# Kernel tuning notes

Hardware: AMD Instinct MI355X
Metric: run time of the kernel (lower is better)

Reference implementation:

```python
import jax, jax.numpy as jnp
import numpy as np

B, LQ, LK = 4, 512, 512
QS, KS, H, DV = 512, 512, 256, 512


def setup_inputs() -> dict:
    key = jax.random.key(0)
    ks = jax.random.split(key, 9)
    s_q = 1.0 / np.sqrt(QS)
    s_k = 1.0 / np.sqrt(KS)
    s_v = 1.0 / np.sqrt(H)
    return {
        "query": jax.random.normal(ks[0], (B, LQ, QS), jnp.float32),
        "key": jax.random.normal(ks[1], (B, LK, KS), jnp.float32),
        "value": jax.random.normal(ks[2], (B, LK, DV), jnp.float32),
        "wq": jax.random.uniform(ks[3], (H, QS), jnp.float32, -s_q, s_q),
        "bq": jax.random.uniform(ks[4], (H,), jnp.float32, -s_q, s_q),
        "wk": jax.random.uniform(ks[5], (H, KS), jnp.float32, -s_k, s_k),
        "bk": jax.random.uniform(ks[6], (H,), jnp.float32, -s_k, s_k),
        "wv": jax.random.uniform(ks[7], (H,), jnp.float32, -s_v, s_v),
        "bv": jax.random.uniform(ks[8], (), jnp.float32, -s_v, s_v),
    }


def reference(query, key, value, wq, bq, wk, bk, wv, bv):
    # q: [B, Lq, H], k: [B, Lk, H]
    q = jnp.einsum('bqd,hd->bqh', query, wq) + bq
    k = jnp.einsum('bkd,hd->bkh', key, wk) + bk
    # broadcast add -> [B, Lq, Lk, H], tanh, project to scalar score
    feats = jnp.tanh(q[:, :, None, :] + k[:, None, :, :])
    scores = jnp.einsum('bqkh,h->bqk', feats, wv) + bv  # [B, Lq, Lk]
    attn = jax.nn.softmax(scores, axis=-1)
    # dropout p=0.0 (identity at inference)
    return jnp.einsum('bqk,bkd->bqd', attn, value)
```

## Files before the change

### kernel.cpp

```cpp
#include <hip/hip_runtime.h>

#define LOG2E 1.4426950408889634f

constexpr int Bb = 4, LQ = 512, LK = 512, QS = 512, H = 256, DV = 512;
constexpr int M = 2048;

constexpr size_t OFF_EQT = 0;
constexpr size_t OFF_EKT = 2u << 20;
constexpr size_t OFF_PQ  = 4u << 20;
constexpr size_t OFF_ROW = 6u << 20;

using bf16x8 = __attribute__((ext_vector_type(8))) short;
using f32x4v = __attribute__((ext_vector_type(4))) float;

__device__ inline unsigned short f2bf(float x) {
    unsigned int u = __float_as_uint(x);
    u += 0x7FFFu + ((u >> 16) & 1u);
    return (unsigned short)(u >> 16);
}
__device__ inline unsigned int pk2(float lo, float hi) {
    return (unsigned int)f2bf(lo) | ((unsigned int)f2bf(hi) << 16);
}

__global__ __launch_bounds__(256) void proj_mfma(
    const float* __restrict__ query, const float* __restrict__ key,
    const float* __restrict__ wq, const float* __restrict__ wk,
    const float* __restrict__ bq, const float* __restrict__ bk,
    char* __restrict__ ws, float scale)
{
    const int z = blockIdx.z;
    const float* A    = z ? key : query;
    const float* W    = z ? wk : wq;
    const float* bias = z ? bk : bq;
    float* out = (float*)(ws + (z ? OFF_EKT : OFF_EQT));

    __shared__ unsigned short Als[64][136];
    __shared__ unsigned short Wls[64][136];
    __shared__ float Ot[64][68];

    const int mb = blockIdx.x * 64, nb = blockIdx.y * 64;
    const int tid = threadIdx.x;
    const int wid = tid >> 6, lane = tid & 63;
    const int ml = lane & 15, quad = lane >> 4;

    f32x4v acc[4] = {{0,0,0,0},{0,0,0,0},{0,0,0,0},{0,0,0,0}};

    for (int kc = 0; kc < QS; kc += 128) {
        __syncthreads();
#pragma unroll
        for (int it = 0; it < 4; ++it) {
            int u = tid + it * 256;
            int row = u >> 4, c8 = (u & 15) * 8;
            float4 a0 = *(const float4*)(A + (size_t)(mb + row) * 512 + kc + c8);
            float4 a1 = *(const float4*)(A + (size_t)(mb + row) * 512 + kc + c8 + 4);
            uint4 pa = { pk2(a0.x, a0.y), pk2(a0.z, a0.w), pk2(a1.x, a1.y), pk2(a1.z, a1.w) };
            *(uint4*)&Als[row][c8] = pa;
            float4 w0 = *(const float4*)(W + (size_t)(nb + row) * 512 + kc + c8);
            float4 w1 = *(const float4*)(W + (size_t)(nb + row) * 512 + kc + c8 + 4);
            uint4 pw = { pk2(w0.x, w0.y), pk2(w0.z, w0.w), pk2(w1.x, w1.y), pk2(w1.z, w1.w) };
            *(uint4*)&Wls[row][c8] = pw;
        }
        __syncthreads();
#pragma unroll
        for (int s = 0; s < 4; ++s) {
            int k = s * 32 + quad * 8;
            bf16x8 af = *(const bf16x8*)&Als[wid * 16 + ml][k];
#pragma unroll
            for (int nt = 0; nt < 4; ++nt) {
                bf16x8 bfr = *(const bf16x8*)&Wls[nt * 16 + ml][k];
                acc[nt] = __builtin_amdgcn_mfma_f32_16x16x32_bf16(af, bfr, acc[nt], 0, 0, 0);
            }
        }
    }
    __syncthreads();
#pragma unroll
    for (int nt = 0; nt < 4; ++nt)
#pragma unroll
        for (int r = 0; r < 4; ++r)
            Ot[nt * 16 + ml][wid * 16 + quad * 4 + r] = acc[nt][r];
    __syncthreads();
    {
        int r0 = tid >> 2;
        int c0 = (tid & 3) * 16;
        float bs = bias[nb + r0];
#pragma unroll
        for (int g = 0; g < 4; ++g) {
            float4 v = *(const float4*)&Ot[r0][c0 + g * 4];
            float4 o;
            o.x = __builtin_amdgcn_exp2f(fminf(fmaxf(scale * (v.x + bs), -15.f), 15.f));
            o.y = __builtin_amdgcn_exp2f(fminf(fmaxf(scale * (v.y + bs), -15.f), 15.f));
            o.z = __builtin_amdgcn_exp2f(fminf(fmaxf(scale * (v.z + bs), -15.f), 15.f));
            o.w = __builtin_amdgcn_exp2f(fminf(fmaxf(scale * (v.w + bs), -15.f), 15.f));
            *(float4*)(out + (size_t)(nb + r0) * 2048 + mb + c0 + g * 4) = o;
        }
    }
}

__global__ __launch_bounds__(256, 1) void score_kernel(
    const float* __restrict__ wvp, char* __restrict__ ws)
{
    const float* EqT = (const float*)(ws + OFF_EQT);
    const float* EkT = (const float*)(ws + OFF_EKT);
    unsigned short* Pq = (unsigned short*)(ws + OFF_PQ);
    float* rowpart = (float*)(ws + OFF_ROW);

    __shared__ float Qs[64][64];
    __shared__ float Ks[64][64];
    __shared__ float Wv2[H];
    __shared__ float redS[4][64];

    const int b  = blockIdx.z;
    const int qb = blockIdx.x * 64;
    const int kt = blockIdx.y;
    const int kb = kt * 64;
    const int tid = threadIdx.x;
    const int tx = tid & 15;
    const int ty = tid >> 4;
    const int w  = tid >> 6;
    const int lane = tid & 63;

    Wv2[tid] = wvp[tid] * (2.0f * LOG2E);

    const int mq = b * LQ + qb;
    const int mk = b * LK + kb;
    const int sh = tid >> 4;
    const int sm = (tid & 15) * 4;

    float acc[4][4] = {};

    for (int h0 = 0; h0 < H; h0 += 64) {
        __syncthreads();
#pragma unroll
        for (int it = 0; it < 4; ++it) {
            int h = sh + 16 * it;
            *(float4*)&Qs[h][sm] = *(const float4*)(EqT + (size_t)(h0 + h) * M + mq + sm);
            *(float4*)&Ks[h][sm] = *(const float4*)(EkT + (size_t)(h0 + h) * M + mk + sm);
        }
        __syncthreads();
#pragma unroll 4
        for (int hh = 0; hh < 64; hh += 4) {
            float4 q1 = *(const float4*)&Qs[hh][tx * 4];
            float4 q2 = *(const float4*)&Qs[hh + 1][tx * 4];
            float4 q3 = *(const float4*)&Qs[hh + 2][tx * 4];
            float4 q4 = *(const float4*)&Qs[hh + 3][tx * 4];
            float4 k1 = *(const float4*)&Ks[hh][ty * 4];
            float4 k2 = *(const float4*)&Ks[hh + 1][ty * 4];
            float4 k3 = *(const float4*)&Ks[hh + 2][ty * 4];
            float4 k4 = *(const float4*)&Ks[hh + 3][ty * 4];
            float4 w4v = *(const float4*)&Wv2[h0 + hh];
            const float w1 = w4v.x, w2 = w4v.y, w3 = w4v.z, w4 = w4v.w;
            const float q1a[4] = {q1.x, q1.y, q1.z, q1.w};
            const float q2a[4] = {q2.x, q2.y, q2.z, q2.w};
            const float q3a[4] = {q3.x, q3.y, q3.z, q3.w};
            const float q4a[4] = {q4.x, q4.y, q4.z, q4.w};
            const float k1a[4] = {k1.x, k1.y, k1.z, k1.w};
            const float k2a[4] = {k2.x, k2.y, k2.z, k2.w};
            const float k3a[4] = {k3.x, k3.y, k3.z, k3.w};
            const float k4a[4] = {k4.x, k4.y, k4.z, k4.w};
#pragma unroll
            for (int i = 0; i < 4; ++i)
#pragma unroll
                for (int j = 0; j < 4; ++j) {
                    float ta = fmaf(q1a[i], k1a[j], 1.0f);
                    float tb = fmaf(q2a[i], k2a[j], 1.0f);
                    float tc = fmaf(q3a[i], k3a[j], 1.0f);
                    float td = fmaf(q4a[i], k4a[j], 1.0f);
                    float t12 = ta * tb;
                    float t34 = tc * td;
                    float n12 = fmaf(w1, tb, w2 * ta);
                    float n34 = fmaf(w3, td, w4 * tc);
                    float num = fmaf(n12, t34, n34 * t12);
                    float den = t12 * t34;
                    acc[i][j] = fmaf(num, __builtin_amdgcn_rcpf(den), acc[i][j]);
                }
        }
    }

    float ps[4];
#pragma unroll
    for (int i = 0; i < 4; ++i) {
        int q = qb + tx * 4 + i;
        float p0 = __builtin_amdgcn_exp2f(-acc[i][0]);
        float p1 = __builtin_amdgcn_exp2f(-acc[i][1]);
        float p2 = __builtin_amdgcn_exp2f(-acc[i][2]);
        float p3 = __builtin_amdgcn_exp2f(-acc[i][3]);
        ps[i] = (p0 + p1) + (p2 + p3);
        uint2 o = { pk2(p0, p1), pk2(p2, p3) };
        *(uint2*)(Pq + ((size_t)(b * 512 + q) * 512 + kb + ty * 4)) = o;
    }
#pragma unroll
    for (int i = 0; i < 4; ++i) {
        ps[i] += __shfl_xor(ps[i], 16, 64);
        ps[i] += __shfl_xor(ps[i], 32, 64);
    }
    if (lane < 16) {
#pragma unroll
        for (int i = 0; i < 4; ++i) redS[w][tx * 4 + i] = ps[i];
    }
    __syncthreads();
    if (tid < 64) {
        float s = (redS[0][tid] + redS[1][tid]) + (redS[2][tid] + redS[3][tid]);
        rowpart[(size_t)kt * 2048 + b * 512 + qb + tid] = s;
    }
}

__global__ __launch_bounds__(256) void av_mfma(
    const float* __restrict__ V, const char* __restrict__ wsc,
    float* __restrict__ O)
{
    const unsigned short* Pq = (const unsigned short*)(wsc + OFF_PQ);
    const float* rowpart = (const float*)(wsc + OFF_ROW);

    __shared__ unsigned short Pls[64][136];
    __shared__ unsigned short Vls[64][136];

    const int b = blockIdx.z, qb = blockIdx.x * 64, nb = blockIdx.y * 64;
    const int tid = threadIdx.x;
    const int wid = tid >> 6, lane = tid & 63;
    const int ml = lane & 15, quad = lane >> 4;
    const unsigned short* Pb = Pq + (size_t)b * 512 * 512;
    const float* Vb = V + (size_t)b * 512 * 512;

    f32x4v acc[4] = {{0,0,0,0},{0,0,0,0},{0,0,0,0},{0,0,0,0}};

    for (int kc = 0; kc < LK; kc += 128) {
        __syncthreads();
#pragma unroll
        for (int it = 0; it < 4; ++it) {
            int u = tid + it * 256;
            int row = u >> 4, c8 = (u & 15) * 8;
            *(uint4*)&Pls[row][c8] = *(const uint4*)(Pb + (size_t)(qb + row) * 512 + kc + c8);
        }
#pragma unroll
        for (int it = 0; it < 8; ++it) {
            int u = tid + it * 256;
            int k = u >> 4, c4 = (u & 15) * 4;
            float4 v4 = *(const float4*)(Vb + (size_t)(kc + k) * 512 + nb + c4);
            Vls[c4 + 0][k] = f2bf(v4.x);
            Vls[c4 + 1][k] = f2bf(v4.y);
            Vls[c4 + 2][k] = f2bf(v4.z);
            Vls[c4 + 3][k] = f2bf(v4.w);
        }
        __syncthreads();
#pragma unroll
        for (int s = 0; s < 4; ++s) {
            int k = s * 32 + quad * 8;
            bf16x8 af = *(const bf16x8*)&Pls[wid * 16 + ml][k];
#pragma unroll
            for (int nt = 0; nt < 4; ++nt) {
                bf16x8 bfr = *(const bf16x8*)&Vls[nt * 16 + ml][k];
                acc[nt] = __builtin_amdgcn_mfma_f32_16x16x32_bf16(af, bfr, acc[nt], 0, 0, 0);
            }
        }
    }

    float rr[4];
#pragma unroll
    for (int r = 0; r < 4; ++r) {
        int q = qb + wid * 16 + quad * 4 + r;
        float rs = 0.f;
#pragma unroll
        for (int t = 0; t < 8; ++t) rs += rowpart[(size_t)t * 2048 + b * 512 + q];
        rr[r] = 1.0f / rs;
    }
#pragma unroll
    for (int nt = 0; nt < 4; ++nt)
#pragma unroll
        for (int r = 0; r < 4; ++r) {
            int q = qb + wid * 16 + quad * 4 + r;
            O[((size_t)b * 512 + q) * 512 + nb + nt * 16 + ml] = acc[nt][r] * rr[r];
        }
}

extern "C" void kernel_launch(void* const* d_in, const int* in_sizes, int n_in,
                              void* d_out, int out_size, void* d_ws, size_t ws_size,
                              hipStream_t stream) {
    const float* query = (const float*)d_in[0];
    const float* key   = (const float*)d_in[1];
    const float* value = (const float*)d_in[2];
    const float* wq    = (const float*)d_in[3];
    const float* bq    = (const float*)d_in[4];
    const float* wk    = (const float*)d_in[5];
    const float* bk    = (const float*)d_in[6];
    const float* wv    = (const float*)d_in[7];
    float* out = (float*)d_out;
    char* ws = (char*)d_ws;

    const float c2 = 2.0f * LOG2E;

    proj_mfma<<<dim3(32, 4, 2), 256, 0, stream>>>(query, key, wq, wk, bq, bk, ws, c2);
    score_kernel<<<dim3(8, 8, Bb), 256, 0, stream>>>(wv, ws);
    av_mfma<<<dim3(8, 8, Bb), 256, 0, stream>>>(value, ws, out);
}
```

Baseline: 138.2 us.

## Double threads per block in score/AV kernels and pre-transpose V to bf16

The score kernel now runs 512 threads per block, with each thread computing a 4x2 micro-tile instead of 4x4. This halves per-thread work and register pressure and raises the number of active waves on a grid of only 256 blocks. A new vconv kernel converts V to bf16 and transposes it once into the workspace, so av_mfma can load V tiles with plain vector copies instead of scattered per-element transposing LDS stores. av_mfma also uses 512 threads with each wave computing two N-tiles, and pk2 uses the hardware packed bf16 convert instruction. The cost is an extra kernel launch and an extra global round-trip for the bf16 copy of V.

```diff
diff --git a/kernel.cpp b/kernel.cpp
--- a/kernel.cpp
+++ b/kernel.cpp
@@ -9,6 +9,7 @@
 constexpr size_t OFF_EKT = 2u << 20;
 constexpr size_t OFF_PQ  = 4u << 20;
 constexpr size_t OFF_ROW = 6u << 20;
+constexpr size_t OFF_VT  = 8u << 20;
 
 using bf16x8 = __attribute__((ext_vector_type(8))) short;
 using f32x4v = __attribute__((ext_vector_type(4))) float;
@@ -19,7 +20,9 @@
     return (unsigned short)(u >> 16);
 }
 __device__ inline unsigned int pk2(float lo, float hi) {
-    return (unsigned int)f2bf(lo) | ((unsigned int)f2bf(hi) << 16);
+    unsigned int r;
+    asm("v_cvt_pk_bf16_f32 %0, %1, %2" : "=v"(r) : "v"(lo), "v"(hi));
+    return r;
 }
 
 __global__ __launch_bounds__(256) void proj_mfma(
@@ -96,7 +99,35 @@
     }
 }
 
-__global__ __launch_bounds__(256, 1) void score_kernel(
+__global__ __launch_bounds__(256) void vconv(
+    const float* __restrict__ V, char* __restrict__ ws)
+{
+    unsigned short* VT = (unsigned short*)(ws + OFF_VT);
+    __shared__ unsigned short T[64][72];
+    const int b = blockIdx.z, k0 = blockIdx.x * 64, n0 = blockIdx.y * 64;
+    const int tid = threadIdx.x;
+    const float* Vb = V + (size_t)b * 512 * 512;
+    const int r = tid >> 4, c = (tid & 15) * 4;
+#pragma unroll
+    for (int it = 0; it < 4; ++it) {
+        int kr = r + it * 16;
+        float4 v = *(const float4*)(Vb + (size_t)(k0 + kr) * 512 + n0 + c);
+        T[c + 0][kr] = f2bf(v.x);
+        T[c + 1][kr] = f2bf(v.y);
+        T[c + 2][kr] = f2bf(v.z);
+        T[c + 3][kr] = f2bf(v.w);
+    }
+    __syncthreads();
+    const int rowO = tid >> 3, colO = (tid & 7) * 8;
+#pragma unroll
+    for (int it = 0; it < 2; ++it) {
+        int n = rowO + it * 32;
+        uint4 o = *(const uint4*)&T[n][colO];
+        *(uint4*)(VT + ((size_t)b * 512 + n0 + n) * 512 + k0 + colO) = o;
+    }
+}
+
+__global__ __launch_bounds__(512, 2) void score_kernel(
     const float* __restrict__ wvp, char* __restrict__ ws)
 {
     const float* EqT = (const float*)(ws + OFF_EQT);
@@ -107,7 +138,7 @@
     __shared__ float Qs[64][64];
     __shared__ float Ks[64][64];
     __shared__ float Wv2[H];
-    __shared__ float redS[4][64];
+    __shared__ float redS[8][64];
 
     const int b  = blockIdx.z;
     const int qb = blockIdx.x * 64;
@@ -119,20 +150,20 @@
     const int w  = tid >> 6;
     const int lane = tid & 63;
 
-    Wv2[tid] = wvp[tid] * (2.0f * LOG2E);
+    if (tid < H) Wv2[tid] = wvp[tid] * (2.0f * LOG2E);
 
     const int mq = b * LQ + qb;
     const int mk = b * LK + kb;
     const int sh = tid >> 4;
     const int sm = (tid & 15) * 4;
 
-    float acc[4][4] = {};
+    float acc[4][2] = {};
 
     for (int h0 = 0; h0 < H; h0 += 64) {
         __syncthreads();
 #pragma unroll
-        for (int it = 0; it < 4; ++it) {
-            int h = sh + 16 * it;
+        for (int it = 0; it < 2; ++it) {
+            int h = sh + 32 * it;
             *(float4*)&Qs[h][sm] = *(const float4*)(EqT + (size_t)(h0 + h) * M + mq + sm);
             *(float4*)&Ks[h][sm] = *(const float4*)(EkT + (size_t)(h0 + h) * M + mk + sm);
         }
@@ -143,24 +174,24 @@
             float4 q2 = *(const float4*)&Qs[hh + 1][tx * 4];
             float4 q3 = *(const float4*)&Qs[hh + 2][tx * 4];
             float4 q4 = *(const float4*)&Qs[hh + 3][tx * 4];
-            float4 k1 = *(const float4*)&Ks[hh][ty * 4];
-            float4 k2 = *(const float4*)&Ks[hh + 1][ty * 4];
-            float4 k3 = *(const float4*)&Ks[hh + 2][ty * 4];
-            float4 k4 = *(const float4*)&Ks[hh + 3][ty * 4];
+            float2 k1 = *(const float2*)&Ks[hh][ty * 2];
+            float2 k2 = *(const float2*)&Ks[hh + 1][ty * 2];
+            float2 k3 = *(const float2*)&Ks[hh + 2][ty * 2];
+            float2 k4 = *(const float2*)&Ks[hh + 3][ty * 2];
             float4 w4v = *(const float4*)&Wv2[h0 + hh];
             const float w1 = w4v.x, w2 = w4v.y, w3 = w4v.z, w4 = w4v.w;
             const float q1a[4] = {q1.x, q1.y, q1.z, q1.w};
             const float q2a[4] = {q2.x, q2.y, q2.z, q2.w};
             const float q3a[4] = {q3.x, q3.y, q3.z, q3.w};
             const float q4a[4] = {q4.x, q4.y, q4.z, q4.w};
-            const float k1a[4] = {k1.x, k1.y, k1.z, k1.w};
-            const float k2a[4] = {k2.x, k2.y, k2.z, k2.w};
-            const float k3a[4] = {k3.x, k3.y, k3.z, k3.w};
-            const float k4a[4] = {k4.x, k4.y, k4.z, k4.w};
+            const float k1a[2] = {k1.x, k1.y};
+            const float k2a[2] = {k2.x, k2.y};
+            const float k3a[2] = {k3.x, k3.y};
+            const float k4a[2] = {k4.x, k4.y};
 #pragma unroll
             for (int i = 0; i < 4; ++i)
 #pragma unroll
-                for (int j = 0; j < 4; ++j) {
+                for (int j = 0; j < 2; ++j) {
                     float ta = fmaf(q1a[i], k1a[j], 1.0f);
                     float tb = fmaf(q2a[i], k2a[j], 1.0f);
                     float tc = fmaf(q3a[i], k3a[j], 1.0f);
@@ -182,11 +213,8 @@
         int q = qb + tx * 4 + i;
         float p0 = __builtin_amdgcn_exp2f(-acc[i][0]);
         float p1 = __builtin_amdgcn_exp2f(-acc[i][1]);
-        float p2 = __builtin_amdgcn_exp2f(-acc[i][2]);
-        float p3 = __builtin_amdgcn_exp2f(-acc[i][3]);
-        ps[i] = (p0 + p1) + (p2 + p3);
-        uint2 o = { pk2(p0, p1), pk2(p2, p3) };
-        *(uint2*)(Pq + ((size_t)(b * 512 + q) * 512 + kb + ty * 4)) = o;
+        ps[i] = p0 + p1;
+        *(unsigned int*)(Pq + ((size_t)(b * 512 + q) * 512 + kb + ty * 2)) = pk2(p0, p1);
     }
 #pragma unroll
     for (int i = 0; i < 4; ++i) {
@@ -199,16 +227,17 @@
     }
     __syncthreads();
     if (tid < 64) {
-        float s = (redS[0][tid] + redS[1][tid]) + (redS[2][tid] + redS[3][tid]);
+        float s = ((redS[0][tid] + redS[1][tid]) + (redS[2][tid] + redS[3][tid]))
+                + ((redS[4][tid] + redS[5][tid]) + (redS[6][tid] + redS[7][tid]));
         rowpart[(size_t)kt * 2048 + b * 512 + qb + tid] = s;
     }
 }
 
-__global__ __launch_bounds__(256) void av_mfma(
-    const float* __restrict__ V, const char* __restrict__ wsc,
-    float* __restrict__ O)
+__global__ __launch_bounds__(512, 2) void av_mfma(
+    const char* __restrict__ wsc, float* __restrict__ O)
 {
     const unsigned short* Pq = (const unsigned short*)(wsc + OFF_PQ);
+    const unsigned short* VT = (const unsigned short*)(wsc + OFF_VT);
     const float* rowpart = (const float*)(wsc + OFF_ROW);
 
     __shared__ unsigned short Pls[64][136];
@@ -218,38 +247,30 @@
     const int tid = threadIdx.x;
     const int wid = tid >> 6, lane = tid & 63;
     const int ml = lane & 15, quad = lane >> 4;
+    const int ms = wid & 3, nh = wid >> 2;
     const unsigned short* Pb = Pq + (size_t)b * 512 * 512;
-    const float* Vb = V + (size_t)b * 512 * 512;
-
-    f32x4v acc[4] = {{0,0,0,0},{0,0,0,0},{0,0,0,0},{0,0,0,0}};
+    const unsigned short* Vb = VT + (size_t)b * 512 * 512;
+
+    f32x4v acc[2] = {{0,0,0,0},{0,0,0,0}};
 
     for (int kc = 0; kc < LK; kc += 128) {
         __syncthreads();
 #pragma unroll
-        for (int it = 0; it < 4; ++it) {
-            int u = tid + it * 256;
+        for (int it = 0; it < 2; ++it) {
+            int u = tid + it * 512;
             int row = u >> 4, c8 = (u & 15) * 8;
             *(uint4*)&Pls[row][c8] = *(const uint4*)(Pb + (size_t)(qb + row) * 512 + kc + c8);
-        }
-#pragma unroll
-        for (int it = 0; it < 8; ++it) {
-            int u = tid + it * 256;
-            int k = u >> 4, c4 = (u & 15) * 4;
-            float4 v4 = *(const float4*)(Vb + (size_t)(kc + k) * 512 + nb + c4);
-            Vls[c4 + 0][k] = f2bf(v4.x);
-            Vls[c4 + 1][k] = f2bf(v4.y);
-            Vls[c4 + 2][k] = f2bf(v4.z);
-            Vls[c4 + 3][k] = f2bf(v4.w);
+            *(uint4*)&Vls[row][c8] = *(const uint4*)(Vb + (size_t)(nb + row) * 512 + kc + c8);
         }
         __syncthreads();
 #pragma unroll
         for (int s = 0; s < 4; ++s) {
             int k = s * 32 + quad * 8;
-            bf16x8 af = *(const bf16x8*)&Pls[wid * 16 + ml][k];
-#pragma unroll
-            for (int nt = 0; nt < 4; ++nt) {
-                bf16x8 bfr = *(const bf16x8*)&Vls[nt * 16 + ml][k];
-                acc[nt] = __builtin_amdgcn_mfma_f32_16x16x32_bf16(af, bfr, acc[nt], 0, 0, 0);
+            bf16x8 af = *(const bf16x8*)&Pls[ms * 16 + ml][k];
+#pragma unroll
+            for (int t = 0; t < 2; ++t) {
+                bf16x8 bfr = *(const bf16x8*)&Vls[(nh * 2 + t) * 16 + ml][k];
+                acc[t] = __builtin_amdgcn_mfma_f32_16x16x32_bf16(af, bfr, acc[t], 0, 0, 0);
             }
         }
     }
@@ -257,18 +278,18 @@
     float rr[4];
 #pragma unroll
     for (int r = 0; r < 4; ++r) {
-        int q = qb + wid * 16 + quad * 4 + r;
+        int q = qb + ms * 16 + quad * 4 + r;
         float rs = 0.f;
 #pragma unroll
-        for (int t = 0; t < 8; ++t) rs += rowpart[(size_t)t * 2048 + b * 512 + q];
+        for (int t8 = 0; t8 < 8; ++t8) rs += rowpart[(size_t)t8 * 2048 + b * 512 + q];
         rr[r] = 1.0f / rs;
     }
 #pragma unroll
-    for (int nt = 0; nt < 4; ++nt)
+    for (int t = 0; t < 2; ++t)
 #pragma unroll
         for (int r = 0; r < 4; ++r) {
-            int q = qb + wid * 16 + quad * 4 + r;
-            O[((size_t)b * 512 + q) * 512 + nb + nt * 16 + ml] = acc[nt][r] * rr[r];
+            int q = qb + ms * 16 + quad * 4 + r;
+            O[((size_t)b * 512 + q) * 512 + nb + (nh * 2 + t) * 16 + ml] = acc[t][r] * rr[r];
         }
 }
 
@@ -289,6 +310,7 @@
     const float c2 = 2.0f * LOG2E;
 
     proj_mfma<<<dim3(32, 4, 2), 256, 0, stream>>>(query, key, wq, wk, bq, bk, ws, c2);
-    score_kernel<<<dim3(8, 8, Bb), 256, 0, stream>>>(wv, ws);
-    av_mfma<<<dim3(8, 8, Bb), 256, 0, stream>>>(value, ws, out);
-}
+    vconv<<<dim3(8, 8, Bb), 256, 0, stream>>>(value, ws);
+    score_kernel<<<dim3(8, 8, Bb), 512, 0, stream>>>(wv, ws);
+    av_mfma<<<dim3(8, 8, Bb), 512, 0, stream>>>(ws, out);
+}
```

Result: faster. 118.9 us (-13.9%).
